# Optimization experiments

Hardware: AMD Instinct MI355X
Metric: run time of the kernel (lower is better)

Reference implementation:

```python
import jax, jax.numpy as jnp
import numpy as np

ATOM_FDIM = 39
BOND_FDIM = 11
MAX_NB = 6
N_ATOMS = 100_000
N_BONDS = 200_001  # index 0 is the padding bond
N_MOLS = 1000
HIDDEN = 256
DEPTH = 6


def setup_inputs() -> dict:
    key = jax.random.key(0)
    ks = jax.random.split(key, 8)
    fatoms = jax.random.normal(ks[0], (N_ATOMS, ATOM_FDIM), dtype=jnp.float32)
    fbonds = jax.random.normal(ks[1], (N_BONDS, ATOM_FDIM + BOND_FDIM), dtype=jnp.float32)
    fbonds = fbonds.at[0].set(0.0)  # padding bond has zero features, as in tensorize()
    agraph = jax.random.randint(ks[2], (N_ATOMS, MAX_NB), 0, N_BONDS, dtype=jnp.int64 if jax.config.jax_enable_x64 else jnp.int32)
    bgraph = jax.random.randint(ks[3], (N_BONDS, MAX_NB), 0, N_BONDS, dtype=agraph.dtype)
    bgraph = bgraph.at[0].set(0)
    mol_ids = jnp.sort(jax.random.randint(ks[4], (N_ATOMS,), 0, N_MOLS, dtype=agraph.dtype))
    scale_i = 1.0 / np.sqrt(ATOM_FDIM + BOND_FDIM)
    scale_h = 1.0 / np.sqrt(HIDDEN)
    scale_o = 1.0 / np.sqrt(ATOM_FDIM + HIDDEN)
    W_i = jax.random.normal(ks[5], (HIDDEN, ATOM_FDIM + BOND_FDIM), dtype=jnp.float32) * scale_i
    W_h = jax.random.normal(ks[6], (HIDDEN, HIDDEN), dtype=jnp.float32) * scale_h
    W_o = jax.random.normal(ks[7], (HIDDEN, ATOM_FDIM + HIDDEN), dtype=jnp.float32) * scale_o
    b_o = jnp.zeros((HIDDEN,), dtype=jnp.float32)
    return {
        'fatoms': fatoms, 'fbonds': fbonds, 'agraph': agraph, 'bgraph': bgraph,
        'mol_ids': mol_ids, 'n_mols': N_MOLS, 'depth': DEPTH,
        'W_i': W_i, 'W_h': W_h, 'W_o': W_o, 'b_o': b_o,
    }


def reference(fatoms, fbonds, agraph, bgraph, mol_ids, n_mols, depth, W_i, W_h, W_o, b_o):
    # binput: [E, H]; message passing over directed bond graph
    binput = fbonds @ W_i.T
    message = jax.nn.relu(binput)
    for _ in range(depth - 1):
        nei = message[bgraph].sum(axis=1)          # [E, MAX_NB, H] gather -> [E, H]
        message = jax.nn.relu(binput + nei @ W_h.T)
    nei = message[agraph].sum(axis=1)              # [N, H]
    ainput = jnp.concatenate([fatoms, nei], axis=1)
    atom_hiddens = jax.nn.relu(ainput @ W_o.T + b_o)  # [N, H]
    # per-molecule mean (equivalent to the scope-based slicing mean)
    sums = jax.ops.segment_sum(atom_hiddens, mol_ids, num_segments=n_mols)
    counts = jax.ops.segment_sum(jnp.ones((atom_hiddens.shape[0],), dtype=atom_hiddens.dtype), mol_ids, num_segments=n_mols)
    mol_vecs = sums / jnp.maximum(counts, 1.0)[:, None]
    return mol_vecs
```

## Files before the change

### kernel.cpp

```cpp
#include <hip/hip_runtime.h>

#define HID 256
#define AS_LD 72
#define TB_LD 264

typedef unsigned short u16;
typedef unsigned int u32;
typedef short bf16x8 __attribute__((ext_vector_type(8)));
typedef float f32x4 __attribute__((ext_vector_type(4)));
typedef u16 u16x8 __attribute__((ext_vector_type(8)));

static __device__ __forceinline__ float bf2f(u16 b) {
    u32 u = ((u32)b) << 16;
    return __uint_as_float(u);
}
static __device__ __forceinline__ u16 f2bf(float f) {
    u32 u = __float_as_uint(f);
    return (u16)((u + 0x7FFFu + ((u >> 16) & 1u)) >> 16);
}

__global__ __launch_bounds__(512, 4) void fused_layer(
    const u16* __restrict__ Sg, const int* __restrict__ graph, int c1,
    const u16* __restrict__ Bd, int ldbd, int c2,
    const float* __restrict__ Cf, int ldcf, int Kc, int c3,
    const u16* __restrict__ WB, int ldw,
    const float* __restrict__ bias,
    u16* __restrict__ C, int M)
{
    __shared__ __align__(16) u16 lds[32 * TB_LD];
    u16* As = lds;

    const int t    = threadIdx.x;
    const int w    = t >> 6;
    const int lane = t & 63;
    const int row0 = blockIdx.x * 64;
    const int wc   = w * 32;
    const int fr   = lane & 15;
    const int fq   = lane >> 4;

    const int g  = t & 7;
    const int ra = t >> 3;

    int nbi[6];
    const u16* bdp = nullptr;
    {
        const int gr = row0 + ra;
        if (c1 > 0) {
            const int* gp = graph + (size_t)(gr < M ? gr : 0) * 6;
            #pragma unroll
            for (int j = 0; j < 6; ++j) nbi[j] = __builtin_nontemporal_load(&gp[j]);
        }
        if (c2 > 0) bdp = Bd + (size_t)(gr < M ? gr : 0) * ldbd;
    }

    f32x4 acc[4][2] = {};
    const int nch = c1 + c2 + c3;
    const int nbf = c1 + c2;

    #pragma unroll 1
    for (int kc = 0; kc < nch; ++kc) {
        __syncthreads();
        if (kc < c1) {
            u16x8 v[6];
            #pragma unroll
            for (int j = 0; j < 6; ++j)
                v[j] = *(const u16x8*)(Sg + (size_t)nbi[j] * 256 + kc * 64 + g * 8);
            float sa[8] = {};
            #pragma unroll
            for (int j = 0; j < 6; ++j)
                #pragma unroll
                for (int e = 0; e < 8; ++e) sa[e] += bf2f(v[j][e]);
            u16x8 o;
            #pragma unroll
            for (int e = 0; e < 8; ++e) o[e] = f2bf(sa[e]);
            *(u16x8*)(As + ra * AS_LD + g * 8) = o;
        } else if (kc < nbf) {
            const u16x8 v = __builtin_nontemporal_load(
                (const u16x8*)(bdp + (kc - c1) * 64 + g * 8));
            *(u16x8*)(As + ra * AS_LD + g * 8) = v;
        } else {
            const int kb = (kc - nbf) * 64;
            const int gr = row0 + ra;
            u16 tmp[8];
            #pragma unroll
            for (int i = 0; i < 8; ++i) {
                const int k = kb + g * 8 + i;
                const float v = (gr < M && k < Kc) ? Cf[(size_t)gr * ldcf + k] : 0.f;
                tmp[i] = f2bf(v);
            }
            *(uint4*)(As + ra * AS_LD + g * 8) = *(const uint4*)tmp;
        }
        __syncthreads();

        #pragma unroll
        for (int s = 0; s < 2; ++s) {
            bf16x8 bq[2];
            #pragma unroll
            for (int j = 0; j < 2; ++j) {
                const int col = wc + j * 16 + fr;
                bq[j] = *(const bf16x8*)(WB + (size_t)col * ldw + kc * 64 + s * 32 + fq * 8);
            }
            bf16x8 af[4];
            #pragma unroll
            for (int i = 0; i < 4; ++i)
                af[i] = *(const bf16x8*)(As + (i * 16 + fr) * AS_LD + s * 32 + fq * 8);
            #pragma unroll
            for (int j = 0; j < 2; ++j)
                #pragma unroll
                for (int i = 0; i < 4; ++i)
                    acc[i][j] = __builtin_amdgcn_mfma_f32_16x16x32_bf16(bq[j], af[i], acc[i][j], 0, 0, 0);
        }
    }

    u16* Tb = lds;
    #pragma unroll
    for (int s2 = 0; s2 < 2; ++s2) {
        __syncthreads();
        #pragma unroll
        for (int j = 0; j < 2; ++j) {
            const int gc = wc + j * 16 + fq * 4;
            float4 bv = make_float4(0.f, 0.f, 0.f, 0.f);
            if (bias) bv = *(const float4*)&bias[gc];
            #pragma unroll
            for (int ii = 0; ii < 2; ++ii) {
                const int i = s2 * 2 + ii;
                u16 o[4];
                o[0] = f2bf(fmaxf(acc[i][j][0] + bv.x, 0.f));
                o[1] = f2bf(fmaxf(acc[i][j][1] + bv.y, 0.f));
                o[2] = f2bf(fmaxf(acc[i][j][2] + bv.z, 0.f));
                o[3] = f2bf(fmaxf(acc[i][j][3] + bv.w, 0.f));
                *(uint2*)(Tb + (ii * 16 + fr) * TB_LD + gc) = *(const uint2*)o;
            }
        }
        __syncthreads();
        const int gsl = t & 31;
        const int rb  = t >> 5;
        #pragma unroll
        for (int it2 = 0; it2 < 2; ++it2) {
            const int rl = it2 * 16 + rb;
            const int gr = row0 + s2 * 32 + rl;
            if (gr < M) {
                const u16x8 v = *(const u16x8*)(Tb + rl * TB_LD + gsl * 8);
                __builtin_nontemporal_store(v, (u16x8*)(C + (size_t)gr * 256 + gsl * 8));
            }
        }
    }
}

__global__ void build_wb(const float* __restrict__ src1, int lds1, int off1, int k1,
                         const float* __restrict__ src2, int lds2, int off2, int k2,
                         u16* __restrict__ dst, int ldd)
{
    const int n = blockIdx.x;
    for (int k = threadIdx.x; k < ldd; k += blockDim.x) {
        float v = 0.f;
        if (k < k1)           v = src1[(size_t)n * lds1 + off1 + k];
        else if (k < k1 + k2) v = src2[(size_t)n * lds2 + off2 + (k - k1)];
        dst[(size_t)n * ldd + k] = f2bf(v);
    }
}

__global__ void build_fb(const float* __restrict__ fb, u16* __restrict__ FB, int E)
{
    const int e = blockIdx.x * 4 + (threadIdx.x >> 6);
    if (e >= E) return;
    const int k = threadIdx.x & 63;
    FB[(size_t)e * 64 + k] = (k < 50) ? f2bf(fb[(size_t)e * 50 + k]) : (u16)0;
}

__global__ void segment_mean(const u16* __restrict__ atomh, const int* __restrict__ mol_ids,
                             float* __restrict__ out, int N)
{
    const int m = blockIdx.x;
    const int t = threadIdx.x;
    __shared__ int s_lo, s_hi;
    if (t == 0) {
        int lo = 0, hi = N;
        while (lo < hi) { int mid = (lo + hi) >> 1; if (mol_ids[mid] < m) lo = mid + 1; else hi = mid; }
        s_lo = lo;
        lo = s_lo; hi = N;
        while (lo < hi) { int mid = (lo + hi) >> 1; if (mol_ids[mid] < m + 1) lo = mid + 1; else hi = mid; }
        s_hi = lo;
    }
    __syncthreads();
    const int lo = s_lo, hi = s_hi;
    float sum = 0.f;
    for (int a = lo; a < hi; ++a) sum += bf2f(atomh[(size_t)a * HID + t]);
    const float cnt = (float)((hi - lo) > 1 ? (hi - lo) : 1);
    out[(size_t)m * HID + t] = sum / cnt;
}

extern "C" void kernel_launch(void* const* d_in, const int* in_sizes, int n_in,
                              void* d_out, int out_size, void* d_ws, size_t ws_size,
                              hipStream_t stream)
{
    const float* fatoms = (const float*)d_in[0];
    const float* fbonds = (const float*)d_in[1];
    const int*   agraph = (const int*)d_in[2];
    const int*   bgraph = (const int*)d_in[3];
    const int*   mol_ids = (const int*)d_in[4];
    const float* W_i = (const float*)d_in[7];
    const float* W_h = (const float*)d_in[8];
    const float* W_o = (const float*)d_in[9];
    const float* b_o = (const float*)d_in[10];

    const int N = in_sizes[0] / 39;
    const int E = in_sizes[1] / 50;
    const int N_MOLS = 1000;
    const int DEPTH = 6;

    const size_t EH = (size_t)E * HID;
    const size_t wbh_sz = (size_t)256 * 320;
    const size_t wbi_sz = (size_t)256 * 64;
    const size_t wbo_sz = (size_t)256 * 320;
    const size_t wsz = wbh_sz + wbi_sz + wbo_sz;
    const size_t fb_sz = (size_t)E * 64;

    const size_t need_nofb = (2 * EH + wsz) * sizeof(u16);
    const size_t need_fb   = (2 * EH + fb_sz + wsz) * sizeof(u16);
    if (ws_size < need_nofb) return;
    const bool use_fb = (ws_size >= need_fb);

    u16* buf0 = (u16*)d_ws;
    u16* buf1 = buf0 + EH;
    u16* FB   = use_fb ? (buf1 + EH) : nullptr;
    u16* wbh  = (use_fb ? FB + fb_sz : buf1 + EH);
    u16* wbi  = wbh + wbh_sz;
    u16* wbo  = wbi + wbi_sz;

    float* out = (float*)d_out;

    build_wb<<<dim3(256), dim3(64), 0, stream>>>(W_h, 256, 0, 256, W_i, 50, 0, 50, wbh, 320);
    build_wb<<<dim3(256), dim3(64), 0, stream>>>(W_i, 50, 0, 50, W_i, 50, 0, 0, wbi, 64);
    build_wb<<<dim3(256), dim3(64), 0, stream>>>(W_o, 295, 39, 256, W_o, 295, 0, 39, wbo, 320);
    if (use_fb)
        build_fb<<<dim3((E + 3) / 4), dim3(256), 0, stream>>>(fbonds, FB, E);

    const int gE = (E + 63) / 64;
    const int gN = (N + 63) / 64;

    if (use_fb)
        fused_layer<<<dim3(gE), dim3(512), 0, stream>>>(
            nullptr, nullptr, 0, FB, 64, 1, nullptr, 0, 0, 0, wbi, 64, nullptr, buf0, E);
    else
        fused_layer<<<dim3(gE), dim3(512), 0, stream>>>(
            nullptr, nullptr, 0, nullptr, 0, 0, fbonds, 50, 50, 1, wbi, 64, nullptr, buf0, E);

    u16* src = buf0;
    u16* dst = buf1;
    for (int it = 0; it < DEPTH - 1; ++it) {
        if (use_fb)
            fused_layer<<<dim3(gE), dim3(512), 0, stream>>>(
                src, bgraph, 4, FB, 64, 1, nullptr, 0, 0, 0, wbh, 320, nullptr, dst, E);
        else
            fused_layer<<<dim3(gE), dim3(512), 0, stream>>>(
                src, bgraph, 4, nullptr, 0, 0, fbonds, 50, 50, 1, wbh, 320, nullptr, dst, E);
        u16* tmp = src; src = dst; dst = tmp;
    }

    fused_layer<<<dim3(gN), dim3(512), 0, stream>>>(
        src, agraph, 4, nullptr, 0, 0, fatoms, 39, 39, 1, wbo, 320, b_o, dst, N);

    segment_mean<<<dim3(N_MOLS), dim3(256), 0, stream>>>(dst, mol_ids, out, N);
}
```

Baseline: 1.031 ms.

## Stage whole A tile in LDS upfront and drop per-chunk barriers

Instead of filling one 64-column LDS chunk and syncing twice per K-chunk, the kernel now gathers and sums all neighbor messages for its row into a full-width LDS tile before a single barrier. Each thread then handles 32 contiguous columns, with the next neighbor's loads issued while the current one is being added. After that, the MFMA loop runs over LDS with no barriers. The aim is more memory-level parallelism in the gather and less synchronization. In exchange, LDS per block grows to about 42KB, which may cut blocks per CU below the launch-bounds target, and register pressure rises from the 32-float accumulator. The gather path also assumes c1 covers exactly 256 columns.

Measured after the change: 1.268 ms. 1.23x slower.

```diff
diff --git a/kernel.cpp b/kernel.cpp
--- a/kernel.cpp
+++ b/kernel.cpp
@@ -1,7 +1,7 @@
 #include <hip/hip_runtime.h>
 
 #define HID 256
-#define AS_LD 72
+#define AS_LD 328
 #define TB_LD 264
 
 typedef unsigned short u16;
@@ -27,8 +27,7 @@
     const float* __restrict__ bias,
     u16* __restrict__ C, int M)
 {
-    __shared__ __align__(16) u16 lds[32 * TB_LD];
-    u16* As = lds;
+    __shared__ __align__(16) u16 lds[64 * AS_LD];
 
     const int t    = threadIdx.x;
     const int w    = t >> 6;
@@ -40,47 +39,59 @@
 
     const int g  = t & 7;
     const int ra = t >> 3;
-
-    int nbi[6];
-    const u16* bdp = nullptr;
-    {
-        const int gr = row0 + ra;
-        if (c1 > 0) {
-            const int* gp = graph + (size_t)(gr < M ? gr : 0) * 6;
-            #pragma unroll
-            for (int j = 0; j < 6; ++j) nbi[j] = __builtin_nontemporal_load(&gp[j]);
-        }
-        if (c2 > 0) bdp = Bd + (size_t)(gr < M ? gr : 0) * ldbd;
-    }
-
-    f32x4 acc[4][2] = {};
-    const int nch = c1 + c2 + c3;
-    const int nbf = c1 + c2;
-
-    #pragma unroll 1
-    for (int kc = 0; kc < nch; ++kc) {
-        __syncthreads();
-        if (kc < c1) {
-            u16x8 v[6];
-            #pragma unroll
-            for (int j = 0; j < 6; ++j)
-                v[j] = *(const u16x8*)(Sg + (size_t)nbi[j] * 256 + kc * 64 + g * 8);
-            float sa[8] = {};
-            #pragma unroll
-            for (int j = 0; j < 6; ++j)
+    const int gr = row0 + ra;
+    u16* Ar = lds + ra * AS_LD;
+
+    if (c1 > 0) {
+        int nbi[6];
+        const int* gp = graph + (size_t)(gr < M ? gr : 0) * 6;
+        #pragma unroll
+        for (int j = 0; j < 6; ++j) nbi[j] = __builtin_nontemporal_load(&gp[j]);
+
+        const int cb = g * 32;
+        float sa[32];
+        #pragma unroll
+        for (int e = 0; e < 32; ++e) sa[e] = 0.f;
+
+        u16x8 cur[4], nxt[4];
+        {
+            const u16* p = Sg + (size_t)nbi[0] * 256 + cb;
+            #pragma unroll
+            for (int q = 0; q < 4; ++q) cur[q] = *(const u16x8*)(p + q * 8);
+        }
+        #pragma unroll
+        for (int j = 0; j < 6; ++j) {
+            if (j < 5) {
+                const u16* p = Sg + (size_t)nbi[j + 1] * 256 + cb;
                 #pragma unroll
-                for (int e = 0; e < 8; ++e) sa[e] += bf2f(v[j][e]);
-            u16x8 o;
-            #pragma unroll
-            for (int e = 0; e < 8; ++e) o[e] = f2bf(sa[e]);
-            *(u16x8*)(As + ra * AS_LD + g * 8) = o;
-        } else if (kc < nbf) {
+                for (int q = 0; q < 4; ++q) nxt[q] = *(const u16x8*)(p + q * 8);
+            }
+            #pragma unroll
+            for (int q = 0; q < 4; ++q)
+                #pragma unroll
+                for (int e = 0; e < 8; ++e) sa[q * 8 + e] += bf2f(cur[q][e]);
+            #pragma unroll
+            for (int q = 0; q < 4; ++q) cur[q] = nxt[q];
+        }
+        #pragma unroll
+        for (int q = 0; q < 4; ++q) {
+            u16 o[8];
+            #pragma unroll
+            for (int e = 0; e < 8; ++e) o[e] = f2bf(sa[q * 8 + e]);
+            *(uint4*)(Ar + cb + q * 8) = *(const uint4*)o;
+        }
+    }
+    if (c2 > 0) {
+        const u16* bdp = Bd + (size_t)(gr < M ? gr : 0) * ldbd;
+        for (int c = 0; c < c2; ++c) {
             const u16x8 v = __builtin_nontemporal_load(
-                (const u16x8*)(bdp + (kc - c1) * 64 + g * 8));
-            *(u16x8*)(As + ra * AS_LD + g * 8) = v;
-        } else {
-            const int kb = (kc - nbf) * 64;
-            const int gr = row0 + ra;
+                (const u16x8*)(bdp + c * 64 + g * 8));
+            *(u16x8*)(Ar + (c1 + c) * 64 + g * 8) = v;
+        }
+    }
+    if (c3 > 0) {
+        for (int c = 0; c < c3; ++c) {
+            const int kb = c * 64;
             u16 tmp[8];
             #pragma unroll
             for (int i = 0; i < 8; ++i) {
@@ -88,10 +99,14 @@
                 const float v = (gr < M && k < Kc) ? Cf[(size_t)gr * ldcf + k] : 0.f;
                 tmp[i] = f2bf(v);
             }
-            *(uint4*)(As + ra * AS_LD + g * 8) = *(const uint4*)tmp;
-        }
-        __syncthreads();
-
+            *(uint4*)(Ar + (c1 + c2 + c) * 64 + g * 8) = *(const uint4*)tmp;
+        }
+    }
+    __syncthreads();
+
+    const int nch = c1 + c2 + c3;
+    f32x4 acc[4][2] = {};
+    for (int kc = 0; kc < nch; ++kc) {
         #pragma unroll
         for (int s = 0; s < 2; ++s) {
             bf16x8 bq[2];
@@ -103,7 +118,7 @@
             bf16x8 af[4];
             #pragma unroll
             for (int i = 0; i < 4; ++i)
-                af[i] = *(const bf16x8*)(As + (i * 16 + fr) * AS_LD + s * 32 + fq * 8);
+                af[i] = *(const bf16x8*)(lds + (i * 16 + fr) * AS_LD + kc * 64 + s * 32 + fq * 8);
             #pragma unroll
             for (int j = 0; j < 2; ++j)
                 #pragma unroll
@@ -138,10 +153,10 @@
         #pragma unroll
         for (int it2 = 0; it2 < 2; ++it2) {
             const int rl = it2 * 16 + rb;
-            const int gr = row0 + s2 * 32 + rl;
-            if (gr < M) {
+            const int grr = row0 + s2 * 32 + rl;
+            if (grr < M) {
                 const u16x8 v = *(const u16x8*)(Tb + rl * TB_LD + gsl * 8);
-                __builtin_nontemporal_store(v, (u16x8*)(C + (size_t)gr * 256 + gsl * 8));
+                __builtin_nontemporal_store(v, (u16x8*)(C + (size_t)grr * 256 + gsl * 8));
             }
         }
     }
```

## Double-buffer LDS tile and prefetch next chunk's gather into registers

Applied to the files above, without the earlier changes.

The A-tile staging moves to two LDS buffers. Each iteration first writes the previously loaded chunk, then issues the global gather loads for the next chunk before the MFMA work. The two `__syncthreads` per chunk become one `s_waitcnt` plus `s_barrier`, so gather latency from the neighbour-sum loads can overlap with matrix multiply. The cost is more live registers (six 8-wide vectors or eight floats held across the MFMA loop) under a 512x4 launch bound, which risks spills or lower occupancy.

Result: slower. 1.099 ms (+6.6%).

```diff
diff --git a/kernel.cpp b/kernel.cpp
--- a/kernel.cpp
+++ b/kernel.cpp
@@ -27,8 +27,7 @@
     const float* __restrict__ bias,
     u16* __restrict__ C, int M)
 {
-    __shared__ __align__(16) u16 lds[32 * TB_LD];
-    u16* As = lds;
+    __shared__ __align__(16) u16 lds[2 * 64 * AS_LD];
 
     const int t    = threadIdx.x;
     const int w    = t >> 6;
@@ -40,57 +39,69 @@
 
     const int g  = t & 7;
     const int ra = t >> 3;
+    const int gr = row0 + ra;
+    const int grc = gr < M ? gr : 0;
 
     int nbi[6];
     const u16* bdp = nullptr;
-    {
-        const int gr = row0 + ra;
-        if (c1 > 0) {
-            const int* gp = graph + (size_t)(gr < M ? gr : 0) * 6;
-            #pragma unroll
-            for (int j = 0; j < 6; ++j) nbi[j] = __builtin_nontemporal_load(&gp[j]);
-        }
-        if (c2 > 0) bdp = Bd + (size_t)(gr < M ? gr : 0) * ldbd;
-    }
-
-    f32x4 acc[4][2] = {};
+    if (c1 > 0) {
+        const int* gp = graph + (size_t)grc * 6;
+        #pragma unroll
+        for (int j = 0; j < 6; ++j) nbi[j] = __builtin_nontemporal_load(&gp[j]);
+    }
+    if (c2 > 0) bdp = Bd + (size_t)grc * ldbd;
+
     const int nch = c1 + c2 + c3;
     const int nbf = c1 + c2;
 
+    u16x8 va[6];
+    float fa[8];
+
+    auto issue = [&](int kc) {
+        if (kc < c1) {
+            #pragma unroll
+            for (int j = 0; j < 6; ++j)
+                va[j] = *(const u16x8*)(Sg + (size_t)nbi[j] * 256 + kc * 64 + g * 8);
+        } else if (kc < nbf) {
+            va[0] = __builtin_nontemporal_load(
+                (const u16x8*)(bdp + (kc - c1) * 64 + g * 8));
+        } else {
+            const int kb = (kc - nbf) * 64 + g * 8;
+            #pragma unroll
+            for (int i = 0; i < 8; ++i)
+                fa[i] = (gr < M && kb + i < Kc) ? Cf[(size_t)gr * ldcf + kb + i] : 0.f;
+        }
+    };
+
+    auto consume = [&](int kc, u16* Ab) {
+        u16 o[8];
+        if (kc < c1) {
+            float sa[8] = {};
+            #pragma unroll
+            for (int j = 0; j < 6; ++j)
+                #pragma unroll
+                for (int e = 0; e < 8; ++e) sa[e] += bf2f(va[j][e]);
+            #pragma unroll
+            for (int e = 0; e < 8; ++e) o[e] = f2bf(sa[e]);
+        } else if (kc < nbf) {
+            *(u16x8*)o = va[0];
+        } else {
+            #pragma unroll
+            for (int i = 0; i < 8; ++i) o[i] = f2bf(fa[i]);
+        }
+        *(uint4*)(Ab + ra * AS_LD + g * 8) = *(const uint4*)o;
+    };
+
+    f32x4 acc[4][2] = {};
+    issue(0);
     #pragma unroll 1
     for (int kc = 0; kc < nch; ++kc) {
-        __syncthreads();
-        if (kc < c1) {
-            u16x8 v[6];
-            #pragma unroll
-            for (int j = 0; j < 6; ++j)
-                v[j] = *(const u16x8*)(Sg + (size_t)nbi[j] * 256 + kc * 64 + g * 8);
-            float sa[8] = {};
-            #pragma unroll
-            for (int j = 0; j < 6; ++j)
-                #pragma unroll
-                for (int e = 0; e < 8; ++e) sa[e] += bf2f(v[j][e]);
-            u16x8 o;
-            #pragma unroll
-            for (int e = 0; e < 8; ++e) o[e] = f2bf(sa[e]);
-            *(u16x8*)(As + ra * AS_LD + g * 8) = o;
-        } else if (kc < nbf) {
-            const u16x8 v = __builtin_nontemporal_load(
-                (const u16x8*)(bdp + (kc - c1) * 64 + g * 8));
-            *(u16x8*)(As + ra * AS_LD + g * 8) = v;
-        } else {
-            const int kb = (kc - nbf) * 64;
-            const int gr = row0 + ra;
-            u16 tmp[8];
-            #pragma unroll
-            for (int i = 0; i < 8; ++i) {
-                const int k = kb + g * 8 + i;
-                const float v = (gr < M && k < Kc) ? Cf[(size_t)gr * ldcf + k] : 0.f;
-                tmp[i] = f2bf(v);
-            }
-            *(uint4*)(As + ra * AS_LD + g * 8) = *(const uint4*)tmp;
-        }
-        __syncthreads();
+        u16* Ab = lds + (kc & 1) * (64 * AS_LD);
+        consume(kc, Ab);
+        if (kc + 1 < nch) issue(kc + 1);
+        asm volatile("s_waitcnt lgkmcnt(0)" ::: "memory");
+        __builtin_amdgcn_s_barrier();
+        asm volatile("" ::: "memory");
 
         #pragma unroll
         for (int s = 0; s < 2; ++s) {
@@ -103,7 +114,7 @@
             bf16x8 af[4];
             #pragma unroll
             for (int i = 0; i < 4; ++i)
-                af[i] = *(const bf16x8*)(As + (i * 16 + fr) * AS_LD + s * 32 + fq * 8);
+                af[i] = *(const bf16x8*)(Ab + (i * 16 + fr) * AS_LD + s * 32 + fq * 8);
             #pragma unroll
             for (int j = 0; j < 2; ++j)
                 #pragma unroll
@@ -138,10 +149,10 @@
         #pragma unroll
         for (int it2 = 0; it2 < 2; ++it2) {
             const int rl = it2 * 16 + rb;
-            const int gr = row0 + s2 * 32 + rl;
-            if (gr < M) {
+            const int grr = row0 + s2 * 32 + rl;
+            if (grr < M) {
                 const u16x8 v = *(const u16x8*)(Tb + rl * TB_LD + gsl * 8);
-                __builtin_nontemporal_store(v, (u16x8*)(C + (size_t)gr * 256 + gsl * 8));
+                __builtin_nontemporal_store(v, (u16x8*)(C + (size_t)grr * 256 + gsl * 8));
             }
         }
     }
```
